# Kernel optimization log

Hardware: AMD Instinct MI355X
Metric: run time of the kernel (lower is better)

## Reference

```python
import jax, jax.numpy as jnp
import numpy as np

N, E = 50000, 800000
NODE_DIM, EDGE_DIM, HIDDEN = 128, 32, 128


def setup_inputs() -> dict:
    key = jax.random.key(0)
    ks = jax.random.split(key, 12)
    def lin(k, fan_in, shape):
        bound = 1.0 / np.sqrt(fan_in)
        return jax.random.uniform(k, shape, jnp.float32, -bound, bound)
    return {
        "x": jax.random.normal(ks[0], (N, NODE_DIM), jnp.float32),
        "edge_index": jax.random.randint(ks[1], (2, E), 0, N),
        "edge_attr": jax.random.normal(ks[2], (E, EDGE_DIM), jnp.float32),
        # msg MLP: Linear(node+edge -> hidden), Linear(hidden -> hidden)
        "W1": lin(ks[3], NODE_DIM + EDGE_DIM, (HIDDEN, NODE_DIM + EDGE_DIM)),
        "b1": lin(ks[4], NODE_DIM + EDGE_DIM, (HIDDEN,)),
        "W2": lin(ks[5], HIDDEN, (HIDDEN, HIDDEN)),
        "b2": lin(ks[6], HIDDEN, (HIDDEN,)),
        # GRUCell(input=HIDDEN, hidden=NODE_DIM); gate order r,z,n (torch)
        "W_ih": lin(ks[7], NODE_DIM, (3 * NODE_DIM, HIDDEN)),
        "b_ih": lin(ks[8], NODE_DIM, (3 * NODE_DIM,)),
        "W_hh": lin(ks[9], NODE_DIM, (3 * NODE_DIM, NODE_DIM)),
        "b_hh": lin(ks[10], NODE_DIM, (3 * NODE_DIM,)),
    }


def reference(x, edge_index, edge_attr, W1, b1, W2, b2, W_ih, b_ih, W_hh, b_hh):
    src, dst = edge_index[0], edge_index[1]
    # gather + edge MLP: [E, node+edge] -> [E, hidden]
    m_in = jnp.concatenate([x[src], edge_attr], axis=-1)
    h1 = jax.nn.silu(m_in @ W1.T + b1)
    m = jax.nn.silu(h1 @ W2.T + b2)
    # scatter-add messages per destination node
    agg = jax.ops.segment_sum(m, dst, num_segments=x.shape[0])  # [N, hidden]
    # GRUCell: gates in torch order (r, z, n)
    gi = agg @ W_ih.T + b_ih  # [N, 3*node_dim]
    gh = x @ W_hh.T + b_hh
    i_r, i_z, i_n = jnp.split(gi, 3, axis=-1)
    h_r, h_z, h_n = jnp.split(gh, 3, axis=-1)
    r = jax.nn.sigmoid(i_r + h_r)
    z = jax.nn.sigmoid(i_z + h_z)
    n = jnp.tanh(i_n + r * h_n)
    return (1.0 - z) * n + z * x
```

## Files before the change

kernel.cpp:

```cpp
#include <hip/hip_runtime.h>
#include <hip/hip_bf16.h>
#include <cstdint>

typedef __bf16 bf16x8 __attribute__((ext_vector_type(8)));
typedef __bf16 bf16x4 __attribute__((ext_vector_type(4)));
typedef float  f32x4  __attribute__((ext_vector_type(4)));

#define ND 128
#define HID 128

__device__ __forceinline__ f32x4 mfma_bf16(bf16x8 a, bf16x8 b, f32x4 c) {
  return __builtin_amdgcn_mfma_f32_16x16x32_bf16(a, b, c, 0, 0, 0);
}
__device__ __forceinline__ float fast_sigmoid(float x) {
  return __fdividef(1.f, 1.f + __expf(-x));
}
__device__ __forceinline__ float fast_silu(float x) {
  return __fdividef(x, 1.f + __expf(-x));
}
__device__ __forceinline__ float fast_tanh(float x) {
  float cx = fminf(fmaxf(x, -15.f), 15.f);
  float e = __expf(2.f * cx);
  return __fdividef(e - 1.f, e + 1.f);
}

__global__ void cvt_all(const float* __restrict__ s0, __bf16* __restrict__ d0, int c1,
                        const float* __restrict__ s1, __bf16* __restrict__ d1, int c2,
                        const float* __restrict__ s2, __bf16* __restrict__ d2, int c3,
                        const float* __restrict__ s3, __bf16* __restrict__ d3, int c4,
                        const float* __restrict__ s4, __bf16* __restrict__ d4, int c5) {
  int i = blockIdx.x * blockDim.x + threadIdx.x;
  const float* s; __bf16* d; int j;
  if (i < c1)      { s = s0; d = d0; j = i; }
  else if (i < c2) { s = s1; d = d1; j = i - c1; }
  else if (i < c3) { s = s2; d = d2; j = i - c2; }
  else if (i < c4) { s = s3; d = d3; j = i - c3; }
  else if (i < c5) { s = s4; d = d4; j = i - c4; }
  else return;
  const float4* sp = reinterpret_cast<const float4*>(s) + (size_t)j * 2;
  float4 a = sp[0], b = sp[1];
  bf16x8 v;
  v[0] = (__bf16)a.x; v[1] = (__bf16)a.y; v[2] = (__bf16)a.z; v[3] = (__bf16)a.w;
  v[4] = (__bf16)b.x; v[5] = (__bf16)b.y; v[6] = (__bf16)b.z; v[7] = (__bf16)b.w;
  reinterpret_cast<bf16x8*>(d)[j] = v;
}

__global__ void k_hist(const int* __restrict__ dst, int* __restrict__ counts, int E) {
  int e = blockIdx.x * 256 + threadIdx.x;
  if (e < E) atomicAdd(&counts[dst[e]], 1);
}

__global__ void k_blocksum(const int* __restrict__ counts, int* __restrict__ bsum) {
  __shared__ int sd[256];
  int t = threadIdx.x;
  sd[t] = counts[blockIdx.x * 256 + t];
  __syncthreads();
  for (int d = 128; d > 0; d >>= 1) { if (t < d) sd[t] += sd[t + d]; __syncthreads(); }
  if (!t) bsum[blockIdx.x] = sd[0];
}

__global__ void k_scan_bsum(int* __restrict__ bsum, int nb) {
  __shared__ int sd[256];
  int t = threadIdx.x;
  int v = (t < nb) ? bsum[t] : 0;
  sd[t] = v;
  __syncthreads();
  for (int d = 1; d < 256; d <<= 1) {
    int u = (t >= d) ? sd[t - d] : 0;
    __syncthreads();
    sd[t] += u;
    __syncthreads();
  }
  if (t < nb) bsum[t] = sd[t] - v;
}

__global__ void k_scan_write(const int* __restrict__ counts, const int* __restrict__ bsum,
                             int* __restrict__ offsets, int* __restrict__ cursor) {
  __shared__ int sd[256];
  int t = threadIdx.x, b = blockIdx.x;
  int i = b * 256 + t;
  int c = counts[i];
  sd[t] = c;
  __syncthreads();
  for (int d = 1; d < 256; d <<= 1) {
    int u = (t >= d) ? sd[t - d] : 0;
    __syncthreads();
    sd[t] += u;
    __syncthreads();
  }
  int excl = bsum[b] + sd[t] - c;
  offsets[i] = excl;
  cursor[i]  = excl;
  if (b == (int)gridDim.x - 1 && t == 255) offsets[i + 1] = excl + c;
}

__global__ void k_spos(const int* __restrict__ dst, int* __restrict__ cursor,
                       int* __restrict__ spos, int E) {
  int e = blockIdx.x * 256 + threadIdx.x;
  if (e < E) spos[e] = atomicAdd(&cursor[dst[e]], 1);
}

#define TILE_E 64

template <int SORT>
__global__ __launch_bounds__(256) void edge_mlp(
    const __bf16* __restrict__ xb,
    const int*    __restrict__ ei,
    const float*  __restrict__ ea,
    const __bf16* __restrict__ W1b,
    const float*  __restrict__ b1,
    const __bf16* __restrict__ W2b,
    const float*  __restrict__ b2,
    float*  __restrict__ agg,
    __bf16* __restrict__ mbuf,
    const int* __restrict__ spos,
    int E, int ntiles)
{
  __shared__ __bf16 Als[TILE_E * 192];
  __shared__ __bf16 H1[TILE_E * 128];
  __shared__ int sposls[TILE_E];
  char* AlsB = (char*)Als;
  char* H1B  = (char*)H1;

  const int tid = threadIdx.x;
  const int w  = tid >> 6;
  const int l  = tid & 63;
  const int l4 = l >> 4;
  const int lm = l & 15;
  const int jb = w * 32;

  bf16x8 bw1[2][5], bw2[2][4];
#pragma unroll
  for (int jt = 0; jt < 2; ++jt) {
    const int jr = jb + jt * 16 + lm;
#pragma unroll
    for (int kt = 0; kt < 5; ++kt)
      bw1[jt][kt] = *reinterpret_cast<const bf16x8*>(W1b + (size_t)jr * 160 + kt * 32 + l4 * 8);
#pragma unroll
    for (int kt = 0; kt < 4; ++kt)
      bw2[jt][kt] = *reinterpret_cast<const bf16x8*>(W2b + (size_t)jr * 128 + kt * 32 + l4 * 8);
  }
  float4 b1v[2], b2v[2];
#pragma unroll
  for (int jt = 0; jt < 2; ++jt) {
    b1v[jt] = *reinterpret_cast<const float4*>(b1 + jb + jt * 16 + l4 * 4);
    b2v[jt] = *reinterpret_cast<const float4*>(b2 + jb + jt * 16 + l4 * 4);
  }
  const int* srcp = ei;
  const int* dstp = ei + E;

  for (int tile = blockIdx.x; tile < ntiles; tile += gridDim.x) {
    const int e0 = tile * TILE_E;

#pragma unroll
    for (int it = 0; it < 4; ++it) {
      int idx = it * 256 + tid;
      int e = idx >> 4, q = idx & 15;
      int s = srcp[e0 + e];
      bf16x8 v = *reinterpret_cast<const bf16x8*>(xb + (size_t)s * ND + q * 8);
      *reinterpret_cast<bf16x8*>(AlsB + e * 384 + ((q ^ (e & 7)) << 4)) = v;
    }
#pragma unroll
    for (int it = 0; it < 2; ++it) {
      int idx = it * 256 + tid;
      int e = idx >> 3, q = idx & 7;
      float4 v = reinterpret_cast<const float4*>(ea)[(size_t)(e0 + e) * 8 + q];
      bf16x4 h;
      h[0] = (__bf16)v.x; h[1] = (__bf16)v.y; h[2] = (__bf16)v.z; h[3] = (__bf16)v.w;
      int chunk = 16 + (q >> 1);
      *reinterpret_cast<bf16x4*>(AlsB + e * 384 + ((chunk ^ (e & 7)) << 4) + ((q & 1) << 3)) = h;
    }
    if (SORT && tid < TILE_E) sposls[tid] = spos[e0 + tid];
    __syncthreads();

#pragma unroll
    for (int et = 0; et < 4; ++et) {
      const int e = et * 16 + lm;
      const int sw = (lm & 7);
      f32x4 acc0 = {0.f, 0.f, 0.f, 0.f}, acc1 = {0.f, 0.f, 0.f, 0.f};
#pragma unroll
      for (int kt = 0; kt < 5; ++kt) {
        bf16x8 bfrag = *reinterpret_cast<const bf16x8*>(AlsB + e * 384 + (((kt * 4 + l4) ^ sw) << 4));
        acc0 = mfma_bf16(bw1[0][kt], bfrag, acc0);
        acc1 = mfma_bf16(bw1[1][kt], bfrag, acc1);
      }
      bf16x4 h0, h1;
#pragma unroll
      for (int rr = 0; rr < 4; ++rr) {
        h0[rr] = (__bf16)fast_silu(acc0[rr] + (&b1v[0].x)[rr]);
        h1[rr] = (__bf16)fast_silu(acc1[rr] + (&b1v[1].x)[rr]);
      }
      int c0 = (jb >> 3) + (l4 >> 1);
      int inner = (l4 & 1) << 3;
      *reinterpret_cast<bf16x4*>(H1B + e * 256 + ((c0 ^ sw) << 4) + inner) = h0;
      *reinterpret_cast<bf16x4*>(H1B + e * 256 + (((c0 + 2) ^ sw) << 4) + inner) = h1;
    }
    __syncthreads();

#pragma unroll
    for (int et = 0; et < 4; ++et) {
      const int e = et * 16 + lm;
      const int sw = (lm & 7);
      f32x4 acc0 = {0.f, 0.f, 0.f, 0.f}, acc1 = {0.f, 0.f, 0.f, 0.f};
#pragma unroll
      for (int kt = 0; kt < 4; ++kt) {
        bf16x8 bfrag = *reinterpret_cast<const bf16x8*>(H1B + e * 256 + (((kt * 4 + l4) ^ sw) << 4));
        acc0 = mfma_bf16(bw2[0][kt], bfrag, acc0);
        acc1 = mfma_bf16(bw2[1][kt], bfrag, acc1);
      }
      if (SORT) {
        bf16x4 m0, m1;
#pragma unroll
        for (int rr = 0; rr < 4; ++rr) {
          m0[rr] = (__bf16)fast_silu(acc0[rr] + (&b2v[0].x)[rr]);
          m1[rr] = (__bf16)fast_silu(acc1[rr] + (&b2v[1].x)[rr]);
        }
        int sp = sposls[e];
        __bf16* rowp = mbuf + (size_t)sp * HID + jb + l4 * 4;
        *reinterpret_cast<bf16x4*>(rowp)      = m0;
        *reinterpret_cast<bf16x4*>(rowp + 16) = m1;
      } else {
        int d = dstp[e0 + e];
#pragma unroll
        for (int rr = 0; rr < 4; ++rr) {
          atomicAdd(agg + (size_t)d * HID + jb + l4 * 4 + rr,
                    fast_silu(acc0[rr] + (&b2v[0].x)[rr]));
          atomicAdd(agg + (size_t)d * HID + jb + 16 + l4 * 4 + rr,
                    fast_silu(acc1[rr] + (&b2v[1].x)[rr]));
        }
      }
    }
    __syncthreads();
  }
}

__global__ __launch_bounds__(256) void k_aggregate(
    const __bf16* __restrict__ mbuf, const int* __restrict__ offsets,
    __bf16* __restrict__ aggb, int N)
{
  int node = blockIdx.x * 4 + (threadIdx.x >> 6);
  int l = threadIdx.x & 63;
  if (node >= N) return;
  int lo = offsets[node], hi = offsets[node + 1];
  int cnt = hi - lo;
  float s0 = 0.f, s1 = 0.f;
  const uint32_t* p = reinterpret_cast<const uint32_t*>(mbuf) + (size_t)lo * 64 + l;
  int r = 0;
  for (; r + 4 <= cnt; r += 4) {
    uint32_t u0 = p[0], u1 = p[64], u2 = p[128], u3 = p[192];
    p += 256;
    s0 += __uint_as_float(u0 << 16) + __uint_as_float(u1 << 16)
        + __uint_as_float(u2 << 16) + __uint_as_float(u3 << 16);
    s1 += __uint_as_float(u0 & 0xffff0000u) + __uint_as_float(u1 & 0xffff0000u)
        + __uint_as_float(u2 & 0xffff0000u) + __uint_as_float(u3 & 0xffff0000u);
  }
  for (; r < cnt; ++r) {
    uint32_t u = p[0];
    p += 64;
    s0 += __uint_as_float(u << 16);
    s1 += __uint_as_float(u & 0xffff0000u);
  }
  uint32_t o = (uint32_t)__builtin_bit_cast(unsigned short, (__bf16)s0) |
               ((uint32_t)__builtin_bit_cast(unsigned short, (__bf16)s1) << 16);
  reinterpret_cast<uint32_t*>(aggb)[(size_t)node * 64 + l] = o;
}

__global__ __launch_bounds__(512) void gru2(
    const __bf16* __restrict__ aggb,
    const __bf16* __restrict__ xb,
    const float*  __restrict__ x,
    const __bf16* __restrict__ Wih, const float* __restrict__ bih,
    const __bf16* __restrict__ Whh, const float* __restrict__ bhh,
    float* __restrict__ out, int N)
{
  const int tid = threadIdx.x;
  const int w = tid >> 6, l = tid & 63;
  const int l4 = l >> 4, lm = l & 15;
  const int n0 = blockIdx.x * 64;
  const int jb = w * 16;
  const int jr = jb + lm, jz = jr + 128, jn = jr + 256;

  bf16x8 WiR[4], WhR[4], WiZ[4], WhZ[4], WiN[4], WhN[4];
#pragma unroll
  for (int kt = 0; kt < 4; ++kt) {
    int ko = kt * 32 + l4 * 8;
    WiR[kt] = *reinterpret_cast<const bf16x8*>(Wih + (size_t)jr * ND + ko);
    WhR[kt] = *reinterpret_cast<const bf16x8*>(Whh + (size_t)jr * ND + ko);
    WiZ[kt] = *reinterpret_cast<const bf16x8*>(Wih + (size_t)jz * ND + ko);
    WhZ[kt] = *reinterpret_cast<const bf16x8*>(Whh + (size_t)jz * ND + ko);
    WiN[kt] = *reinterpret_cast<const bf16x8*>(Wih + (size_t)jn * ND + ko);
    WhN[kt] = *reinterpret_cast<const bf16x8*>(Whh + (size_t)jn * ND + ko);
  }
  float4 birv, bizv, binv, bhnv;
  {
    int j0 = jb + l4 * 4;
    float4 a = *reinterpret_cast<const float4*>(bih + j0);
    float4 b = *reinterpret_cast<const float4*>(bhh + j0);
    birv = make_float4(a.x + b.x, a.y + b.y, a.z + b.z, a.w + b.w);
    a = *reinterpret_cast<const float4*>(bih + 128 + j0);
    b = *reinterpret_cast<const float4*>(bhh + 128 + j0);
    bizv = make_float4(a.x + b.x, a.y + b.y, a.z + b.z, a.w + b.w);
    binv = *reinterpret_cast<const float4*>(bih + 256 + j0);
    bhnv = *reinterpret_cast<const float4*>(bhh + 256 + j0);
  }

#pragma unroll
  for (int rt = 0; rt < 4; ++rt) {
    const int node = n0 + rt * 16 + lm;
    const bool ok = node < N;
    bf16x8 aA[4], aX[4];
#pragma unroll
    for (int kt = 0; kt < 4; ++kt) {
      int ko = kt * 32 + l4 * 8;
      bf16x8 z8 = {};
      aA[kt] = ok ? *reinterpret_cast<const bf16x8*>(aggb + (size_t)node * ND + ko) : z8;
      aX[kt] = ok ? *reinterpret_cast<const bf16x8*>(xb + (size_t)node * ND + ko) : z8;
    }
    f32x4 aR = {0.f,0.f,0.f,0.f}, aZ = {0.f,0.f,0.f,0.f};
    f32x4 ai = {0.f,0.f,0.f,0.f}, ah = {0.f,0.f,0.f,0.f};
#pragma unroll
    for (int kt = 0; kt < 4; ++kt) {
      aR = mfma_bf16(WiR[kt], aA[kt], aR);
      aR = mfma_bf16(WhR[kt], aX[kt], aR);
      aZ = mfma_bf16(WiZ[kt], aA[kt], aZ);
      aZ = mfma_bf16(WhZ[kt], aX[kt], aZ);
      ai = mfma_bf16(WiN[kt], aA[kt], ai);
      ah = mfma_bf16(WhN[kt], aX[kt], ah);
    }
    if (ok) {
      float4 xv = *reinterpret_cast<const float4*>(x + (size_t)node * ND + jb + l4 * 4);
      float4 ov;
#pragma unroll
      for (int rr = 0; rr < 4; ++rr) {
        float r = fast_sigmoid(aR[rr] + (&birv.x)[rr]);
        float z = fast_sigmoid(aZ[rr] + (&bizv.x)[rr]);
        float n = fast_tanh(ai[rr] + (&binv.x)[rr] + r * (ah[rr] + (&bhnv.x)[rr]));
        (&ov.x)[rr] = (1.f - z) * n + z * (&xv.x)[rr];
      }
      *reinterpret_cast<float4*>(out + (size_t)node * ND + jb + l4 * 4) = ov;
    }
  }
}

extern "C" void kernel_launch(void* const* d_in, const int* in_sizes, int n_in,
                              void* d_out, int out_size, void* d_ws, size_t ws_size,
                              hipStream_t stream) {
  const float* x   = (const float*)d_in[0];
  const int*   ei  = (const int*)d_in[1];
  const float* ea  = (const float*)d_in[2];
  const float* W1  = (const float*)d_in[3];
  const float* b1  = (const float*)d_in[4];
  const float* W2  = (const float*)d_in[5];
  const float* b2  = (const float*)d_in[6];
  const float* Wih = (const float*)d_in[7];
  const float* bih = (const float*)d_in[8];
  const float* Whh = (const float*)d_in[9];
  const float* bhh = (const float*)d_in[10];
  float* out = (float*)d_out;
  const int N = in_sizes[0] / ND;
  const int E = in_sizes[1] / 2;

  const int nb = (N + 255) / 256;
  const int nC = nb * 256;

  char* ws = (char*)d_ws;
  size_t off = 0;
  auto alloc = [&](size_t bytes) -> void* {
    void* p = ws + off;
    off += (bytes + 255) & ~(size_t)255;
    return p;
  };
  __bf16* xb   = (__bf16*)alloc((size_t)N * ND * 2);
  __bf16* aggb = (__bf16*)alloc((size_t)N * ND * 2);
  __bf16* W1b  = (__bf16*)alloc(128 * 160 * 2);
  __bf16* W2b  = (__bf16*)alloc(128 * 128 * 2);
  __bf16* Wihb = (__bf16*)alloc(384 * 128 * 2);
  __bf16* Whhb = (__bf16*)alloc(384 * 128 * 2);
  size_t common_off = off;

  int*    counts  = (int*)alloc((size_t)nC * 4);
  int*    offsets = (int*)alloc((size_t)(nC + 16) * 4);
  int*    cursor  = (int*)alloc((size_t)nC * 4);
  int*    bsum    = (int*)alloc(256 * 4);
  int*    spos    = (int*)alloc((size_t)E * 4);
  __bf16* mbuf    = (__bf16*)alloc((size_t)E * HID * 2);
  size_t need_sort = off;

  bool use_sort = (ws_size >= need_sort);

  const int n8_x = N * ND / 8, n8_1 = 128 * 160 / 8, n8_2 = 128 * 128 / 8, n8_g = 384 * 128 / 8;
  int c1 = n8_x, c2 = c1 + n8_1, c3 = c2 + n8_2, c4 = c3 + n8_g, c5 = c4 + n8_g;
  cvt_all<<<(c5 + 255) / 256, 256, 0, stream>>>(x, xb, c1, W1, W1b, c2, W2, W2b, c3,
                                                Wih, Wihb, c4, Whh, Whhb, c5);

  const int ntiles = E / TILE_E;
  const int* dstp = ei + E;

  if (use_sort) {
    hipMemsetAsync(counts, 0, (size_t)nC * 4, stream);
    k_hist<<<(E + 255) / 256, 256, 0, stream>>>(dstp, counts, E);
    k_blocksum<<<nb, 256, 0, stream>>>(counts, bsum);
    k_scan_bsum<<<1, 256, 0, stream>>>(bsum, nb);
    k_scan_write<<<nb, 256, 0, stream>>>(counts, bsum, offsets, cursor);
    k_spos<<<(E + 255) / 256, 256, 0, stream>>>(dstp, cursor, spos, E);
    edge_mlp<1><<<2500, 256, 0, stream>>>(xb, ei, ea, W1b, b1, W2b, b2,
                                          nullptr, mbuf, spos, E, ntiles);
    k_aggregate<<<(N + 3) / 4, 256, 0, stream>>>(mbuf, offsets, aggb, N);
  } else {
    off = common_off;
    float* aggf = (float*)alloc((size_t)N * ND * 4);
    hipMemsetAsync(aggf, 0, (size_t)N * ND * 4, stream);
    edge_mlp<0><<<2500, 256, 0, stream>>>(xb, ei, ea, W1b, b1, W2b, b2,
                                          aggf, nullptr, nullptr, E, ntiles);
    cvt_all<<<(n8_x + 255) / 256, 256, 0, stream>>>(aggf, aggb, n8_x,
                                                    nullptr, nullptr, n8_x,
                                                    nullptr, nullptr, n8_x,
                                                    nullptr, nullptr, n8_x,
                                                    nullptr, nullptr, n8_x);
  }

  gru2<<<(N + 63) / 64, 512, 0, stream>>>(aggb, xb, x, Wihb, bih, Whhb, bhh, out, N);
}
```

Measured before the change: 378.8 us.

## Use 512-thread edge MLP blocks with 16 output columns per wave

The edge MLP kernel now runs with 512 threads (8 waves), and each wave computes 16 hidden columns instead of 32. This halves the weight fragments each wave keeps in registers and splits the gather loads across more threads, aiming for more waves in flight to hide the random gather latency. The scatter positions are stored in an unused padding slot of the A tile in LDS instead of a separate shared array. The cost is more waves per block contending at the barriers, and each wave issues smaller MFMA chains with less work to amortise the per-tile loads.

```diff
diff --git a/kernel.cpp b/kernel.cpp
--- a/kernel.cpp
+++ b/kernel.cpp
@@ -103,7 +103,7 @@
 #define TILE_E 64
 
 template <int SORT>
-__global__ __launch_bounds__(256) void edge_mlp(
+__global__ __launch_bounds__(512, 6) void edge_mlp(
     const __bf16* __restrict__ xb,
     const int*    __restrict__ ei,
     const float*  __restrict__ ea,
@@ -118,7 +118,6 @@
 {
   __shared__ __bf16 Als[TILE_E * 192];
   __shared__ __bf16 H1[TILE_E * 128];
-  __shared__ int sposls[TILE_E];
   char* AlsB = (char*)Als;
   char* H1B  = (char*)H1;
 
@@ -127,25 +126,20 @@
   const int l  = tid & 63;
   const int l4 = l >> 4;
   const int lm = l & 15;
-  const int jb = w * 32;
-
-  bf16x8 bw1[2][5], bw2[2][4];
-#pragma unroll
-  for (int jt = 0; jt < 2; ++jt) {
-    const int jr = jb + jt * 16 + lm;
+  const int jb = w * 16;
+
+  bf16x8 bw1[5], bw2[4];
+  {
+    const int jr = jb + lm;
 #pragma unroll
     for (int kt = 0; kt < 5; ++kt)
-      bw1[jt][kt] = *reinterpret_cast<const bf16x8*>(W1b + (size_t)jr * 160 + kt * 32 + l4 * 8);
+      bw1[kt] = *reinterpret_cast<const bf16x8*>(W1b + (size_t)jr * 160 + kt * 32 + l4 * 8);
 #pragma unroll
     for (int kt = 0; kt < 4; ++kt)
-      bw2[jt][kt] = *reinterpret_cast<const bf16x8*>(W2b + (size_t)jr * 128 + kt * 32 + l4 * 8);
-  }
-  float4 b1v[2], b2v[2];
-#pragma unroll
-  for (int jt = 0; jt < 2; ++jt) {
-    b1v[jt] = *reinterpret_cast<const float4*>(b1 + jb + jt * 16 + l4 * 4);
-    b2v[jt] = *reinterpret_cast<const float4*>(b2 + jb + jt * 16 + l4 * 4);
-  }
+      bw2[kt] = *reinterpret_cast<const bf16x8*>(W2b + (size_t)jr * 128 + kt * 32 + l4 * 8);
+  }
+  float4 b1v = *reinterpret_cast<const float4*>(b1 + jb + l4 * 4);
+  float4 b2v = *reinterpret_cast<const float4*>(b2 + jb + l4 * 4);
   const int* srcp = ei;
   const int* dstp = ei + E;
 
@@ -153,81 +147,70 @@
     const int e0 = tile * TILE_E;
 
 #pragma unroll
-    for (int it = 0; it < 4; ++it) {
-      int idx = it * 256 + tid;
+    for (int it = 0; it < 2; ++it) {
+      int idx = it * 512 + tid;
       int e = idx >> 4, q = idx & 15;
       int s = srcp[e0 + e];
       bf16x8 v = *reinterpret_cast<const bf16x8*>(xb + (size_t)s * ND + q * 8);
       *reinterpret_cast<bf16x8*>(AlsB + e * 384 + ((q ^ (e & 7)) << 4)) = v;
     }
-#pragma unroll
-    for (int it = 0; it < 2; ++it) {
-      int idx = it * 256 + tid;
-      int e = idx >> 3, q = idx & 7;
+    {
+      int e = tid >> 3, q = tid & 7;
       float4 v = reinterpret_cast<const float4*>(ea)[(size_t)(e0 + e) * 8 + q];
       bf16x4 h;
       h[0] = (__bf16)v.x; h[1] = (__bf16)v.y; h[2] = (__bf16)v.z; h[3] = (__bf16)v.w;
       int chunk = 16 + (q >> 1);
       *reinterpret_cast<bf16x4*>(AlsB + e * 384 + ((chunk ^ (e & 7)) << 4) + ((q & 1) << 3)) = h;
     }
-    if (SORT && tid < TILE_E) sposls[tid] = spos[e0 + tid];
+    if (SORT && tid < TILE_E) {
+      int sp = spos[e0 + tid];
+      *reinterpret_cast<int*>(AlsB + tid * 384 + ((20 ^ (tid & 7)) << 4)) = sp;
+    }
     __syncthreads();
 
 #pragma unroll
     for (int et = 0; et < 4; ++et) {
       const int e = et * 16 + lm;
-      const int sw = (lm & 7);
-      f32x4 acc0 = {0.f, 0.f, 0.f, 0.f}, acc1 = {0.f, 0.f, 0.f, 0.f};
+      const int sw = lm & 7;
+      f32x4 acc = {0.f, 0.f, 0.f, 0.f};
 #pragma unroll
       for (int kt = 0; kt < 5; ++kt) {
         bf16x8 bfrag = *reinterpret_cast<const bf16x8*>(AlsB + e * 384 + (((kt * 4 + l4) ^ sw) << 4));
-        acc0 = mfma_bf16(bw1[0][kt], bfrag, acc0);
-        acc1 = mfma_bf16(bw1[1][kt], bfrag, acc1);
+        acc = mfma_bf16(bw1[kt], bfrag, acc);
       }
-      bf16x4 h0, h1;
-#pragma unroll
-      for (int rr = 0; rr < 4; ++rr) {
-        h0[rr] = (__bf16)fast_silu(acc0[rr] + (&b1v[0].x)[rr]);
-        h1[rr] = (__bf16)fast_silu(acc1[rr] + (&b1v[1].x)[rr]);
-      }
-      int c0 = (jb >> 3) + (l4 >> 1);
+      bf16x4 h0;
+#pragma unroll
+      for (int rr = 0; rr < 4; ++rr)
+        h0[rr] = (__bf16)fast_silu(acc[rr] + (&b1v.x)[rr]);
+      int c0 = w * 2 + (l4 >> 1);
       int inner = (l4 & 1) << 3;
       *reinterpret_cast<bf16x4*>(H1B + e * 256 + ((c0 ^ sw) << 4) + inner) = h0;
-      *reinterpret_cast<bf16x4*>(H1B + e * 256 + (((c0 + 2) ^ sw) << 4) + inner) = h1;
     }
     __syncthreads();
 
 #pragma unroll
     for (int et = 0; et < 4; ++et) {
       const int e = et * 16 + lm;
-      const int sw = (lm & 7);
-      f32x4 acc0 = {0.f, 0.f, 0.f, 0.f}, acc1 = {0.f, 0.f, 0.f, 0.f};
+      const int sw = lm & 7;
+      f32x4 acc = {0.f, 0.f, 0.f, 0.f};
 #pragma unroll
       for (int kt = 0; kt < 4; ++kt) {
         bf16x8 bfrag = *reinterpret_cast<const bf16x8*>(H1B + e * 256 + (((kt * 4 + l4) ^ sw) << 4));
-        acc0 = mfma_bf16(bw2[0][kt], bfrag, acc0);
-        acc1 = mfma_bf16(bw2[1][kt], bfrag, acc1);
+        acc = mfma_bf16(bw2[kt], bfrag, acc);
       }
       if (SORT) {
-        bf16x4 m0, m1;
-#pragma unroll
-        for (int rr = 0; rr < 4; ++rr) {
-          m0[rr] = (__bf16)fast_silu(acc0[rr] + (&b2v[0].x)[rr]);
-          m1[rr] = (__bf16)fast_silu(acc1[rr] + (&b2v[1].x)[rr]);
-        }
-        int sp = sposls[e];
-        __bf16* rowp = mbuf + (size_t)sp * HID + jb + l4 * 4;
-        *reinterpret_cast<bf16x4*>(rowp)      = m0;
-        *reinterpret_cast<bf16x4*>(rowp + 16) = m1;
+        bf16x4 m0;
+#pragma unroll
+        for (int rr = 0; rr < 4; ++rr)
+          m0[rr] = (__bf16)fast_silu(acc[rr] + (&b2v.x)[rr]);
+        int sp = *reinterpret_cast<const int*>(AlsB + e * 384 + ((20 ^ sw) << 4));
+        *reinterpret_cast<bf16x4*>(mbuf + (size_t)sp * HID + jb + l4 * 4) = m0;
       } else {
         int d = dstp[e0 + e];
 #pragma unroll
-        for (int rr = 0; rr < 4; ++rr) {
+        for (int rr = 0; rr < 4; ++rr)
           atomicAdd(agg + (size_t)d * HID + jb + l4 * 4 + rr,
-                    fast_silu(acc0[rr] + (&b2v[0].x)[rr]));
-          atomicAdd(agg + (size_t)d * HID + jb + 16 + l4 * 4 + rr,
-                    fast_silu(acc1[rr] + (&b2v[1].x)[rr]));
-        }
+                    fast_silu(acc[rr] + (&b2v.x)[rr]));
       }
     }
     __syncthreads();
@@ -403,14 +386,14 @@
     k_scan_bsum<<<1, 256, 0, stream>>>(bsum, nb);
     k_scan_write<<<nb, 256, 0, stream>>>(counts, bsum, offsets, cursor);
     k_spos<<<(E + 255) / 256, 256, 0, stream>>>(dstp, cursor, spos, E);
-    edge_mlp<1><<<2500, 256, 0, stream>>>(xb, ei, ea, W1b, b1, W2b, b2,
+    edge_mlp<1><<<2500, 512, 0, stream>>>(xb, ei, ea, W1b, b1, W2b, b2,
                                           nullptr, mbuf, spos, E, ntiles);
     k_aggregate<<<(N + 3) / 4, 256, 0, stream>>>(mbuf, offsets, aggb, N);
   } else {
     off = common_off;
     float* aggf = (float*)alloc((size_t)N * ND * 4);
     hipMemsetAsync(aggf, 0, (size_t)N * ND * 4, stream);
-    edge_mlp<0><<<2500, 256, 0, stream>>>(xb, ei, ea, W1b, b1, W2b, b2,
+    edge_mlp<0><<<2500, 512, 0, stream>>>(xb, ei, ea, W1b, b1, W2b, b2,
                                           aggf, nullptr, nullptr, E, ntiles);
     cvt_all<<<(n8_x + 255) / 256, 256, 0, stream>>>(aggf, aggb, n8_x,
                                                     nullptr, nullptr, n8_x,
```

After: 390.1 us. 1.03x slower.
